# Optimization experiments

Hardware: AMD Instinct MI355X
Metric: run time of the kernel (lower is better)

## Reference

```python
import jax, jax.numpy as jnp
import numpy as np

N = 8192        # nodes
E = 262144      # edges (avg degree 32)
IN_CH = 256
CH = 128
SLOPE = 0.2     # PyG GATv2Conv default negative_slope


def gatv2(x, src, dst, wl, wr, att, b):
    """Single-head GATv2Conv (PyG defaults: share_weights=False, self-loops
    already appended to src/dst). x: [N, in]; wl, wr: [out, in]; att: [out]."""
    xl = x @ wl.T                      # [N, out] source-side transform (x_j)
    xr = x @ wr.T                      # [N, out] target-side transform (x_i)
    # per-edge attention logit: att . LeakyReLU(x_l[src] + x_r[dst])
    e = jax.nn.leaky_relu(xl[src] + xr[dst], SLOPE) @ att   # [E']
    # segment softmax over incoming edges of each target node
    m = jax.ops.segment_max(e, dst, num_segments=N)
    p = jnp.exp(e - m[dst])
    s = jax.ops.segment_sum(p, dst, num_segments=N)
    alpha = p / s[dst]                 # every node has a self-loop -> s > 0
    out = jax.ops.segment_sum(alpha[:, None] * xl[src], dst, num_segments=N)
    return out + b


def setup_inputs() -> dict:
    key = jax.random.key(0)
    ks = jax.random.split(key, 2 + 5 * 3)
    inp = {
        "x": jax.random.normal(ks[0], (N, IN_CH), dtype=jnp.float32),
        "edge_index": jax.random.randint(ks[1], (2, E), 0, N, dtype=jnp.int64),
    }
    dims = [(CH, IN_CH), (2 * CH, CH), (CH, 2 * CH), (CH, 2 * CH), (IN_CH, CH)]
    ki = 2
    for i, (oc, ic) in enumerate(dims, start=1):
        sc = (2.0 / (ic + oc)) ** 0.5  # glorot-ish
        inp[f"w{i}l"] = jax.random.normal(ks[ki], (oc, ic), dtype=jnp.float32) * sc
        inp[f"w{i}r"] = jax.random.normal(ks[ki + 1], (oc, ic), dtype=jnp.float32) * sc
        inp[f"a{i}"] = jax.random.normal(ks[ki + 2], (oc,), dtype=jnp.float32) * sc
        inp[f"b{i}"] = jnp.zeros((oc,), dtype=jnp.float32)
        ki += 3
    return inp


def reference(x, edge_index,
              w1l, w1r, a1, b1,
              w2l, w2r, a2, b2,
              w3l, w3r, a3, b3,
              w4l, w4r, a4, b4,
              w5l, w5r, a5, b5):
    loops = jnp.arange(N, dtype=edge_index.dtype)
    src = jnp.concatenate([edge_index[0], loops])   # add_self_loops=True
    dst = jnp.concatenate([edge_index[1], loops])
    h = jax.nn.relu(gatv2(x, src, dst, w1l, w1r, a1, b1))          # [N, CH]
    z = jax.nn.relu(gatv2(h, src, dst, w2l, w2r, a2, b2))          # [N, 2CH]
    re = jax.nn.relu(gatv2(z, src, dst, w3l, w3r, a3, b3))         # [N, CH]
    recon_edge = jax.nn.sigmoid(re @ re.T)                         # [N, N]
    xd = jax.nn.relu(gatv2(z, src, dst, w4l, w4r, a4, b4))         # [N, CH]
    x_rec = jax.nn.relu(gatv2(xd, src, dst, w5l, w5r, a5, b5))     # [N, IN_CH]
    return recon_edge, x_rec, z
```

## Files before the change

### kernel.cpp

```cpp
#include <hip/hip_runtime.h>
#include <hip/hip_bf16.h>
#include <math.h>

#define N_NODES 8192
#define N_EDGES 262144
#define EP (N_EDGES + N_NODES)
#define SLOPE 0.2f

typedef short bf16x8 __attribute__((ext_vector_type(8)));
typedef short short4v __attribute__((ext_vector_type(4)));
typedef float f32x4 __attribute__((ext_vector_type(4)));

__global__ void detect_i64(const int* __restrict__ raw, int* __restrict__ flag) {
    if (threadIdx.x == 0 && blockIdx.x == 0) {
        int acc = 0;
        for (int i = 0; i < 64; ++i) acc |= raw[2 * i + 1];
        *flag = (acc == 0) ? 1 : 0;
    }
}

__global__ void extract_edges(const int* __restrict__ raw, const int* __restrict__ flag,
                              int* __restrict__ esrc, int* __restrict__ edst) {
    int k = blockIdx.x * blockDim.x + threadIdx.x;
    if (k >= N_EDGES) return;
    if (*flag) {
        esrc[k] = raw[2 * (size_t)k];
        edst[k] = raw[2 * ((size_t)N_EDGES + k)];
    } else {
        esrc[k] = raw[k];
        edst[k] = raw[N_EDGES + k];
    }
}

__global__ void hist_k(const int* __restrict__ edst, int* __restrict__ counts) {
    int k = blockIdx.x * blockDim.x + threadIdx.x;
    if (k >= EP) return;
    int d = (k < N_EDGES) ? edst[k] : (k - N_EDGES);
    atomicAdd(&counts[d], 1);
}

__global__ void scan_k(const int* __restrict__ counts, int* __restrict__ row_ptr) {
    __shared__ int part[256];
    int t = threadIdx.x;
    int base = t * 32;
    int loc[32];
    int s = 0;
    for (int i = 0; i < 32; ++i) { loc[i] = s; s += counts[base + i]; }
    part[t] = s;
    __syncthreads();
    for (int off = 1; off < 256; off <<= 1) {
        int tmp = (t >= off) ? part[t - off] : 0;
        __syncthreads();
        part[t] += tmp;
        __syncthreads();
    }
    int incl = part[t];
    int excl = incl - s;
    for (int i = 0; i < 32; ++i) row_ptr[base + i] = excl + loc[i];
    if (t == 255) row_ptr[N_NODES] = incl;
}

__global__ void scatter_k(const int* __restrict__ esrc, const int* __restrict__ edst,
                          const int* __restrict__ row_ptr, int* __restrict__ cursor,
                          int* __restrict__ ssrc) {
    int k = blockIdx.x * blockDim.x + threadIdx.x;
    if (k >= EP) return;
    int s, d;
    if (k < N_EDGES) { s = esrc[k]; d = edst[k]; }
    else             { s = d = k - N_EDGES; }
    int pos = row_ptr[d] + atomicAdd(&cursor[d], 1);
    ssrc[pos] = s;
}

__global__ void cvt_f32_bf16(const float* __restrict__ in, unsigned short* __restrict__ out, int n) {
    int i = blockIdx.x * blockDim.x + threadIdx.x;
    if (i < n) {
        __hip_bfloat16 h = __float2bfloat16(in[i]);
        out[i] = *(unsigned short*)&h;
    }
}

__global__ void split3(const float* __restrict__ in, short* __restrict__ out, int logK) {
    int K = 1 << logK;
    int total = (N_NODES << logK) >> 2;
    int i = blockIdx.x * blockDim.x + threadIdx.x;
    if (i >= total) return;
    int r = i >> (logK - 2);
    int c4 = (i & ((1 << (logK - 2)) - 1)) << 2;
    f32x4 a = *(const f32x4*)&in[((size_t)r << logK) + c4];
    short4v h4, l4;
#pragma unroll
    for (int j = 0; j < 4; ++j) {
        __hip_bfloat16 hb = __float2bfloat16(a[j]);
        float hf = __bfloat162float(hb);
        __hip_bfloat16 lb = __float2bfloat16(a[j] - hf);
        h4[j] = *(short*)&hb;
        l4[j] = *(short*)&lb;
    }
    size_t ro = (size_t)r * (3 << logK);
    *(short4v*)&out[ro + c4] = h4;
    *(short4v*)&out[ro + K + c4] = l4;
    *(short4v*)&out[ro + 2 * K + c4] = h4;
}

__global__ void prep_w3(const float* __restrict__ wl, const float* __restrict__ wr,
                        short* __restrict__ out, int OC, int logK) {
    int K = 1 << logK;
    int i = blockIdx.x * blockDim.x + threadIdx.x;
    if (i >= ((OC << 1) << logK)) return;
    int r = i >> logK, c = i & (K - 1);
    float a = (r < OC) ? wl[((size_t)r << logK) + c]
                       : wr[((size_t)(r - OC) << logK) + c];
    __hip_bfloat16 hb = __float2bfloat16(a);
    float hf = __bfloat162float(hb);
    __hip_bfloat16 lb = __float2bfloat16(a - hf);
    short hs = *(short*)&hb, lo = *(short*)&lb;
    size_t ro = (size_t)r * 3 * K;
    out[ro + c] = hs;
    out[ro + K + c] = hs;
    out[ro + 2 * K + c] = lo;
}

#if __has_builtin(__builtin_amdgcn_global_load_lds)
#define GL16(gsrc, lbase, lofs)                                                       \
    __builtin_amdgcn_global_load_lds((const __attribute__((address_space(1))) void*)(gsrc), \
                                     (__attribute__((address_space(3))) void*)(lbase), 16, 0, 0)
#else
#define GL16(gsrc, lbase, lofs) (*(bf16x8*)((lbase) + (lofs)) = *(const bf16x8*)(gsrc))
#endif

__global__ __launch_bounds__(256) void gemm_bf16_nt(const short* __restrict__ A3,
                                                    const short* __restrict__ W3,
                                                    float* __restrict__ C,
                                                    int K3, int N2) {
    __shared__ __align__(16) short As[4096];
    __shared__ __align__(16) short Bs[4096];
    int tid = threadIdx.x;
    int gx = gridDim.x;
    int lgx = (gx == 8) ? 3 : 2;
    int orig = blockIdx.x + (blockIdx.y << lgx);
    int nwg = gx << 7;
    int swzb = (orig & 7) * (nwg >> 3) + (orig >> 3);
    int bx = swzb & (gx - 1), by = swzb >> lgx;
    int i0 = by * 64, j0 = bx * 64;

    int wave = tid >> 6, lane = tid & 63;
    int b0 = wave * 1024 + lane * 16;
    int row0 = b0 >> 7;
    int rb0 = b0 & 127;
    int scb = rb0 ^ ((row0 & 7) << 4);
    const short* gA0 = A3 + (size_t)(i0 + row0) * K3 + (scb >> 1);
    const short* gA1 = A3 + (size_t)(i0 + row0 + 32) * K3 + (scb >> 1);
    const short* gB0 = W3 + (size_t)(j0 + row0) * K3 + (scb >> 1);
    const short* gB1 = W3 + (size_t)(j0 + row0 + 32) * K3 + (scb >> 1);
    short* lA0 = As + wave * 512;
    short* lA1 = As + 2048 + wave * 512;
    short* lB0 = Bs + wave * 512;
    short* lB1 = Bs + 2048 + wave * 512;
    int lofs = lane * 8;

    int wr = (wave >> 1) * 32, wc = (wave & 1) * 32;
    int lm = lane & 15, quad = lane >> 4;
    f32x4 acc[2][2] = {};
    for (int k0 = 0; k0 < K3; k0 += 64) {
        GL16(gA0 + k0, lA0, lofs);
        GL16(gA1 + k0, lA1, lofs);
        GL16(gB0 + k0, lB0, lofs);
        GL16(gB1 + k0, lB1, lofs);
        __syncthreads();
#pragma unroll
        for (int ks = 0; ks < 2; ++ks) {
            int kb = ks * 64 + quad * 16;
            bf16x8 a[2], b[2];
#pragma unroll
            for (int u = 0; u < 2; ++u) {
                int r = wr + u * 16 + lm;
                a[u] = *(const bf16x8*)((const char*)As + ((((r << 7) | kb)) ^ ((r & 7) << 4)));
            }
#pragma unroll
            for (int v = 0; v < 2; ++v) {
                int r = wc + v * 16 + lm;
                b[v] = *(const bf16x8*)((const char*)Bs + ((((r << 7) | kb)) ^ ((r & 7) << 4)));
            }
#pragma unroll
            for (int u = 0; u < 2; ++u)
#pragma unroll
                for (int v = 0; v < 2; ++v)
                    acc[u][v] = __builtin_amdgcn_mfma_f32_16x16x32_bf16(a[u], b[v], acc[u][v], 0, 0, 0);
        }
        __syncthreads();
    }
#pragma unroll
    for (int u = 0; u < 2; ++u)
#pragma unroll
        for (int v = 0; v < 2; ++v)
#pragma unroll
            for (int r = 0; r < 4; ++r) {
                int row = i0 + wr + u * 16 + quad * 4 + r;
                int col = j0 + wc + v * 16 + lm;
                C[(size_t)row * N2 + col] = acc[u][v][r];
            }
}

#define LSTR 136

__global__ __launch_bounds__(256) void recon_mfma(const unsigned short* __restrict__ Rb,
                                                  float* __restrict__ C) {
    __shared__ __align__(16) short As[128 * LSTR];
    __shared__ __align__(16) short Bs[128 * LSTR];
    int tid = threadIdx.x;
    int orig = blockIdx.x + blockIdx.y * 64;
    int swzb = (orig & 7) * 512 + (orig >> 3);
    int bx = swzb & 63, by = swzb >> 6;
    int i0 = by * 128, j0 = bx * 128;
    const short* R = (const short*)Rb;
#pragma unroll
    for (int c = 0; c < 8; ++c) {
        int idx = tid + c * 256;
        int row = idx >> 4, col = (idx & 15) * 8;
        *(bf16x8*)(&As[row * LSTR + col]) = *(const bf16x8*)(&R[(size_t)(i0 + row) * 128 + col]);
        *(bf16x8*)(&Bs[row * LSTR + col]) = *(const bf16x8*)(&R[(size_t)(j0 + row) * 128 + col]);
    }
    __syncthreads();
    int wave = tid >> 6, lane = tid & 63;
    int wr = (wave >> 1) * 64, wc = (wave & 1) * 64;
    int lm = lane & 15, quad = lane >> 4;
    f32x4 acc[4][4] = {};
#pragma unroll
    for (int ks = 0; ks < 4; ++ks) {
        int ko = ks * 32 + quad * 8;
        bf16x8 a[4], b[4];
#pragma unroll
        for (int u = 0; u < 4; ++u)
            a[u] = *(const bf16x8*)(&As[(wr + u * 16 + lm) * LSTR + ko]);
#pragma unroll
        for (int v = 0; v < 4; ++v)
            b[v] = *(const bf16x8*)(&Bs[(wc + v * 16 + lm) * LSTR + ko]);
#pragma unroll
        for (int u = 0; u < 4; ++u)
#pragma unroll
            for (int v = 0; v < 4; ++v)
                acc[u][v] = __builtin_amdgcn_mfma_f32_16x16x32_bf16(a[u], b[v], acc[u][v], 0, 0, 0);
    }
#pragma unroll
    for (int u = 0; u < 4; ++u)
#pragma unroll
        for (int v = 0; v < 4; ++v)
#pragma unroll
            for (int r = 0; r < 4; ++r) {
                int row = i0 + wr + u * 16 + quad * 4 + r;
                int col = j0 + wc + v * 16 + lm;
                float val = acc[u][v][r];
                C[(size_t)row * 8192 + col] = 1.0f / (1.0f + __expf(-val));
            }
}

__global__ __launch_bounds__(256) void gat_node256(const int* __restrict__ row_ptr,
                                                   const int* __restrict__ ssrc,
                                                   const float* __restrict__ XLR,
                                                   const float* __restrict__ att,
                                                   const float* __restrict__ bias,
                                                   float* __restrict__ outp) {
    __shared__ float sacc[4][256];
    __shared__ float sm[4], ss[4];
    int d = blockIdx.x, t = threadIdx.x;
    int lane = t & 63, wave = t >> 6;
    int beg = row_ptr[d], end = row_ptr[d + 1];
    f32x4 xr = *(const f32x4*)&XLR[(size_t)d * 512 + 256 + lane * 4];
    f32x4 at = *(const f32x4*)&att[lane * 4];
    float m = -INFINITY, s = 0.0f;
    f32x4 acc = {0.0f, 0.0f, 0.0f, 0.0f};
    for (int p = beg + wave; p < end; p += 4) {
        int si = ssrc[p];
        f32x4 v = *(const f32x4*)&XLR[(size_t)si * 512 + lane * 4];
        float e = 0.0f;
#pragma unroll
        for (int j = 0; j < 4; ++j) {
            float u = v[j] + xr[j];
            u = (u > 0.0f) ? u : SLOPE * u;
            e += u * at[j];
        }
#pragma unroll
        for (int off = 32; off; off >>= 1) e += __shfl_xor(e, off, 64);
        float mn = fmaxf(m, e);
        float f = __expf(m - mn), p0 = __expf(e - mn);
        s = s * f + p0;
#pragma unroll
        for (int j = 0; j < 4; ++j) acc[j] = acc[j] * f + p0 * v[j];
        m = mn;
    }
    *(f32x4*)&sacc[wave][lane * 4] = acc;
    if (lane == 0) { sm[wave] = m; ss[wave] = s; }
    __syncthreads();
    float M = fmaxf(fmaxf(sm[0], sm[1]), fmaxf(sm[2], sm[3]));
    float tot = 0.0f, st = 0.0f;
#pragma unroll
    for (int w = 0; w < 4; ++w) {
        float fw = __expf(sm[w] - M);
        tot += sacc[w][t] * fw;
        st += ss[w] * fw;
    }
    outp[(size_t)d * 256 + t] = fmaxf(tot / st + bias[t], 0.0f);
}

__global__ __launch_bounds__(256) void gat_node128(const int* __restrict__ row_ptr,
                                                   const int* __restrict__ ssrc,
                                                   const float* __restrict__ XLR,
                                                   const float* __restrict__ att,
                                                   const float* __restrict__ bias,
                                                   float* __restrict__ outp) {
    __shared__ float sacc[8][128];
    __shared__ float sm[8], ss[8];
    int d = blockIdx.x, t = threadIdx.x;
    int ln = t & 31, hw = t >> 5;
    int beg = row_ptr[d], end = row_ptr[d + 1];
    f32x4 xr = *(const f32x4*)&XLR[(size_t)d * 256 + 128 + ln * 4];
    f32x4 at = *(const f32x4*)&att[ln * 4];
    float m = -INFINITY, s = 0.0f;
    f32x4 acc = {0.0f, 0.0f, 0.0f, 0.0f};
    for (int p = beg + hw; p < end; p += 8) {
        int si = ssrc[p];
        f32x4 v = *(const f32x4*)&XLR[(size_t)si * 256 + ln * 4];
        float e = 0.0f;
#pragma unroll
        for (int j = 0; j < 4; ++j) {
            float u = v[j] + xr[j];
            u = (u > 0.0f) ? u : SLOPE * u;
            e += u * at[j];
        }
#pragma unroll
        for (int off = 16; off; off >>= 1) e += __shfl_xor(e, off, 32);
        float mn = fmaxf(m, e);
        float f = __expf(m - mn), p0 = __expf(e - mn);
        s = s * f + p0;
#pragma unroll
        for (int j = 0; j < 4; ++j) acc[j] = acc[j] * f + p0 * v[j];
        m = mn;
    }
    *(f32x4*)&sacc[hw][ln * 4] = acc;
    if (ln == 0) { sm[hw] = m; ss[hw] = s; }
    __syncthreads();
    if (t < 128) {
        float M = sm[0];
#pragma unroll
        for (int w = 1; w < 8; ++w) M = fmaxf(M, sm[w]);
        float tot = 0.0f, st = 0.0f;
#pragma unroll
        for (int w = 0; w < 8; ++w) {
            float fw = __expf(sm[w] - M);
            tot += sacc[w][t] * fw;
            st += ss[w] * fw;
        }
        outp[(size_t)d * 128 + t] = fmaxf(tot / st + bias[t], 0.0f);
    }
}

static inline int ceil_div(int a, int b) { return (a + b - 1) / b; }

extern "C" void kernel_launch(void* const* d_in, const int* in_sizes, int n_in,
                              void* d_out, int out_size, void* d_ws, size_t ws_size,
                              hipStream_t stream) {
    const float* x    = (const float*)d_in[0];
    const int*   eraw = (const int*)d_in[1];

    const float* wl[5], *wr[5], *att[5], *bia[5];
    for (int l = 0; l < 5; ++l) {
        wl[l]  = (const float*)d_in[2 + 4 * l + 0];
        wr[l]  = (const float*)d_in[2 + 4 * l + 1];
        att[l] = (const float*)d_in[2 + 4 * l + 2];
        bia[l] = (const float*)d_in[2 + 4 * l + 3];
    }
    const int och[5]  = {128, 256, 128, 128, 256};
    const int logK[5] = {8, 7, 8, 8, 7};

    float* outp  = (float*)d_out;
    float* recon = outp;
    float* xrec  = outp + (size_t)67108864;
    float* zout  = outp + (size_t)69206016;

    float* W = (float*)d_ws;
    float* XLR   = W;
    float* hbuf  = W + 4194304;
    float* rebuf = W + 5242880;
    float* xdbuf = W + 6291456;
    short* A3    = (short*)(W + 7340032);
    short* W3    = (short*)(W + 10485760);
    unsigned short* Rb = (unsigned short*)(W + 10682368);
    int* I       = (int*)(W + 11206656);
    int* counts  = I;
    int* cursor  = I + 8192;
    int* row_ptr = I + 16384;
    int* ssrc    = I + 24577;
    int* esrc    = I + 294913;
    int* edst    = I + 557057;
    int* flag    = I + 819201;

    detect_i64<<<1, 64, 0, stream>>>(eraw, flag);
    extract_edges<<<ceil_div(N_EDGES, 256), 256, 0, stream>>>(eraw, flag, esrc, edst);
    hipMemsetAsync(counts, 0, 2 * 8192 * sizeof(int), stream);
    hist_k<<<ceil_div(EP, 256), 256, 0, stream>>>(edst, counts);
    scan_k<<<1, 256, 0, stream>>>(counts, row_ptr);
    scatter_k<<<ceil_div(EP, 256), 256, 0, stream>>>(esrc, edst, row_ptr, cursor, ssrc);

    const float* lin[5] = {x,    hbuf, zout,  zout,  xdbuf};
    float*       lof[5] = {hbuf, zout, rebuf, xdbuf, xrec };

    for (int l = 0; l < 5; ++l) {
        int lk = logK[l], OC = och[l];
        int N2 = OC << 1, K3 = 3 << lk;

        if (l != 3) {
            int tot = (N_NODES << lk) >> 2;
            split3<<<ceil_div(tot, 256), 256, 0, stream>>>(lin[l], A3, lk);
        }
        prep_w3<<<ceil_div(N2 << lk, 256), 256, 0, stream>>>(wl[l], wr[l], W3, OC, lk);

        dim3 g(N2 / 64, N_NODES / 64);
        gemm_bf16_nt<<<g, 256, 0, stream>>>(A3, W3, XLR, K3, N2);

        if (OC == 128)
            gat_node128<<<N_NODES, 256, 0, stream>>>(row_ptr, ssrc, XLR, att[l], bia[l], lof[l]);
        else
            gat_node256<<<N_NODES, 256, 0, stream>>>(row_ptr, ssrc, XLR, att[l], bia[l], lof[l]);

        if (l == 2) {
            cvt_f32_bf16<<<ceil_div(N_NODES * 128, 256), 256, 0, stream>>>(rebuf, Rb, N_NODES * 128);
            dim3 gr(64, 64);
            recon_mfma<<<gr, 256, 0, stream>>>(Rb, recon);
        }
    }
}
```

Measured before the change: 612.9 us.

## Fuse activation splitting into GAT epilogues, batch weight prep, double-buffer GEMM

Each GAT node kernel now writes the bf16 hi/lo/hi split of its output directly into the next layer's GEMM operand, and the recon bf16 copy. This removes the separate split3 and cvt passes and the fp32 intermediate buffers. Edge extraction is merged with the histogram, and self-loop counts move into the scan. All five weight preps run in one launch up front. The GEMM double-buffers its LDS tiles so the next K-tile load overlaps the MFMAs, and it writes XL and XR as separate arrays. The cost is more complex buffer-lifetime reasoning across layers and more LDS per GEMM block.

```diff
diff --git a/kernel.cpp b/kernel.cpp
--- a/kernel.cpp
+++ b/kernel.cpp
@@ -19,23 +19,21 @@
     }
 }
 
-__global__ void extract_edges(const int* __restrict__ raw, const int* __restrict__ flag,
-                              int* __restrict__ esrc, int* __restrict__ edst) {
+__global__ void extract_hist(const int* __restrict__ raw, const int* __restrict__ flag,
+                             int* __restrict__ esrc, int* __restrict__ edst,
+                             int* __restrict__ counts) {
     int k = blockIdx.x * blockDim.x + threadIdx.x;
     if (k >= N_EDGES) return;
+    int s, d;
     if (*flag) {
-        esrc[k] = raw[2 * (size_t)k];
-        edst[k] = raw[2 * ((size_t)N_EDGES + k)];
+        s = raw[2 * (size_t)k];
+        d = raw[2 * ((size_t)N_EDGES + k)];
     } else {
-        esrc[k] = raw[k];
-        edst[k] = raw[N_EDGES + k];
-    }
-}
-
-__global__ void hist_k(const int* __restrict__ edst, int* __restrict__ counts) {
-    int k = blockIdx.x * blockDim.x + threadIdx.x;
-    if (k >= EP) return;
-    int d = (k < N_EDGES) ? edst[k] : (k - N_EDGES);
+        s = raw[k];
+        d = raw[N_EDGES + k];
+    }
+    esrc[k] = s;
+    edst[k] = d;
     atomicAdd(&counts[d], 1);
 }
 
@@ -45,7 +43,7 @@
     int base = t * 32;
     int loc[32];
     int s = 0;
-    for (int i = 0; i < 32; ++i) { loc[i] = s; s += counts[base + i]; }
+    for (int i = 0; i < 32; ++i) { loc[i] = s; s += counts[base + i] + 1; }
     part[t] = s;
     __syncthreads();
     for (int off = 1; off < 256; off <<= 1) {
@@ -72,14 +70,6 @@
     ssrc[pos] = s;
 }
 
-__global__ void cvt_f32_bf16(const float* __restrict__ in, unsigned short* __restrict__ out, int n) {
-    int i = blockIdx.x * blockDim.x + threadIdx.x;
-    if (i < n) {
-        __hip_bfloat16 h = __float2bfloat16(in[i]);
-        out[i] = *(unsigned short*)&h;
-    }
-}
-
 __global__ void split3(const float* __restrict__ in, short* __restrict__ out, int logK) {
     int K = 1 << logK;
     int total = (N_NODES << logK) >> 2;
@@ -103,19 +93,29 @@
     *(short4v*)&out[ro + 2 * K + c4] = h4;
 }
 
-__global__ void prep_w3(const float* __restrict__ wl, const float* __restrict__ wr,
-                        short* __restrict__ out, int OC, int logK) {
-    int K = 1 << logK;
-    int i = blockIdx.x * blockDim.x + threadIdx.x;
-    if (i >= ((OC << 1) << logK)) return;
-    int r = i >> logK, c = i & (K - 1);
-    float a = (r < OC) ? wl[((size_t)r << logK) + c]
-                       : wr[((size_t)(r - OC) << logK) + c];
+struct WPrep {
+    const float* wl[5];
+    const float* wr[5];
+    int oc[5];
+    int lk[5];
+};
+
+__global__ void prep_w3_all(WPrep P, short* __restrict__ out) {
+    int gid = blockIdx.x * blockDim.x + threadIdx.x;
+    int l = gid >> 16;
+    if (l >= 5) return;
+    int rem = gid & 65535;
+    int lk = P.lk[l], K = 1 << lk;
+    int r = rem >> lk, c = rem & (K - 1);
+    int OC = P.oc[l];
+    const float* w = (r < OC) ? P.wl[l] : P.wr[l];
+    int rr = (r < OC) ? r : r - OC;
+    float a = w[((size_t)rr << lk) + c];
     __hip_bfloat16 hb = __float2bfloat16(a);
     float hf = __bfloat162float(hb);
     __hip_bfloat16 lb = __float2bfloat16(a - hf);
     short hs = *(short*)&hb, lo = *(short*)&lb;
-    size_t ro = (size_t)r * 3 * K;
+    size_t ro = (size_t)l * 196608 + (size_t)r * 3 * K;
     out[ro + c] = hs;
     out[ro + K + c] = hs;
     out[ro + 2 * K + c] = lo;
@@ -131,10 +131,11 @@
 
 __global__ __launch_bounds__(256) void gemm_bf16_nt(const short* __restrict__ A3,
                                                     const short* __restrict__ W3,
-                                                    float* __restrict__ C,
-                                                    int K3, int N2) {
-    __shared__ __align__(16) short As[4096];
-    __shared__ __align__(16) short Bs[4096];
+                                                    float* __restrict__ XL,
+                                                    float* __restrict__ XR,
+                                                    int K3, int N2, int OC) {
+    __shared__ __align__(16) short As[2][4096];
+    __shared__ __align__(16) short Bs[2][4096];
     int tid = threadIdx.x;
     int gx = gridDim.x;
     int lgx = (gx == 8) ? 3 : 2;
@@ -153,21 +154,33 @@
     const short* gA1 = A3 + (size_t)(i0 + row0 + 32) * K3 + (scb >> 1);
     const short* gB0 = W3 + (size_t)(j0 + row0) * K3 + (scb >> 1);
     const short* gB1 = W3 + (size_t)(j0 + row0 + 32) * K3 + (scb >> 1);
-    short* lA0 = As + wave * 512;
-    short* lA1 = As + 2048 + wave * 512;
-    short* lB0 = Bs + wave * 512;
-    short* lB1 = Bs + 2048 + wave * 512;
     int lofs = lane * 8;
+
+#define STAGE(pb, k0s)                                      \
+    do {                                                    \
+        GL16(gA0 + (k0s), &As[pb][wave * 512], lofs);       \
+        GL16(gA1 + (k0s), &As[pb][2048 + wave * 512], lofs);\
+        GL16(gB0 + (k0s), &Bs[pb][wave * 512], lofs);       \
+        GL16(gB1 + (k0s), &Bs[pb][2048 + wave * 512], lofs);\
+    } while (0)
 
     int wr = (wave >> 1) * 32, wc = (wave & 1) * 32;
     int lm = lane & 15, quad = lane >> 4;
     f32x4 acc[2][2] = {};
-    for (int k0 = 0; k0 < K3; k0 += 64) {
-        GL16(gA0 + k0, lA0, lofs);
-        GL16(gA1 + k0, lA1, lofs);
-        GL16(gB0 + k0, lB0, lofs);
-        GL16(gB1 + k0, lB1, lofs);
-        __syncthreads();
+    int nt = K3 >> 6;
+    STAGE(0, 0);
+    int cur = 0;
+    for (int t = 0; t < nt; ++t) {
+        if (t + 1 < nt) {
+            STAGE(cur ^ 1, (t + 1) << 6);
+            asm volatile("s_waitcnt vmcnt(4)" ::: "memory");
+        } else {
+            asm volatile("s_waitcnt vmcnt(0)" ::: "memory");
+        }
+        __builtin_amdgcn_s_barrier();
+        __builtin_amdgcn_sched_barrier(0);
+        const char* Ab = (const char*)&As[cur][0];
+        const char* Bb = (const char*)&Bs[cur][0];
 #pragma unroll
         for (int ks = 0; ks < 2; ++ks) {
             int kb = ks * 64 + quad * 16;
@@ -175,12 +188,12 @@
 #pragma unroll
             for (int u = 0; u < 2; ++u) {
                 int r = wr + u * 16 + lm;
-                a[u] = *(const bf16x8*)((const char*)As + ((((r << 7) | kb)) ^ ((r & 7) << 4)));
+                a[u] = *(const bf16x8*)(Ab + (((r << 7) | kb) ^ ((r & 7) << 4)));
             }
 #pragma unroll
             for (int v = 0; v < 2; ++v) {
                 int r = wc + v * 16 + lm;
-                b[v] = *(const bf16x8*)((const char*)Bs + ((((r << 7) | kb)) ^ ((r & 7) << 4)));
+                b[v] = *(const bf16x8*)(Bb + (((r << 7) | kb) ^ ((r & 7) << 4)));
             }
 #pragma unroll
             for (int u = 0; u < 2; ++u)
@@ -188,8 +201,14 @@
                 for (int v = 0; v < 2; ++v)
                     acc[u][v] = __builtin_amdgcn_mfma_f32_16x16x32_bf16(a[u], b[v], acc[u][v], 0, 0, 0);
         }
-        __syncthreads();
-    }
+        __builtin_amdgcn_sched_barrier(0);
+        __builtin_amdgcn_s_barrier();
+        cur ^= 1;
+    }
+#undef STAGE
+    float* Cb;
+    int col0;
+    if (j0 < OC) { Cb = XL; col0 = j0; } else { Cb = XR; col0 = j0 - OC; }
 #pragma unroll
     for (int u = 0; u < 2; ++u)
 #pragma unroll
@@ -197,8 +216,8 @@
 #pragma unroll
             for (int r = 0; r < 4; ++r) {
                 int row = i0 + wr + u * 16 + quad * 4 + r;
-                int col = j0 + wc + v * 16 + lm;
-                C[(size_t)row * N2 + col] = acc[u][v][r];
+                int col = col0 + wc + v * 16 + lm;
+                Cb[(size_t)row * OC + col] = acc[u][v][r];
             }
 }
 
@@ -257,22 +276,24 @@
 
 __global__ __launch_bounds__(256) void gat_node256(const int* __restrict__ row_ptr,
                                                    const int* __restrict__ ssrc,
-                                                   const float* __restrict__ XLR,
+                                                   const float* __restrict__ XL,
+                                                   const float* __restrict__ XR,
                                                    const float* __restrict__ att,
                                                    const float* __restrict__ bias,
-                                                   float* __restrict__ outp) {
+                                                   float* __restrict__ outf,
+                                                   short* __restrict__ a3) {
     __shared__ float sacc[4][256];
     __shared__ float sm[4], ss[4];
     int d = blockIdx.x, t = threadIdx.x;
     int lane = t & 63, wave = t >> 6;
     int beg = row_ptr[d], end = row_ptr[d + 1];
-    f32x4 xr = *(const f32x4*)&XLR[(size_t)d * 512 + 256 + lane * 4];
+    f32x4 xr = *(const f32x4*)&XR[(size_t)d * 256 + lane * 4];
     f32x4 at = *(const f32x4*)&att[lane * 4];
     float m = -INFINITY, s = 0.0f;
     f32x4 acc = {0.0f, 0.0f, 0.0f, 0.0f};
     for (int p = beg + wave; p < end; p += 4) {
         int si = ssrc[p];
-        f32x4 v = *(const f32x4*)&XLR[(size_t)si * 512 + lane * 4];
+        f32x4 v = *(const f32x4*)&XL[(size_t)si * 256 + lane * 4];
         float e = 0.0f;
 #pragma unroll
         for (int j = 0; j < 4; ++j) {
@@ -300,27 +321,40 @@
         tot += sacc[w][t] * fw;
         st += ss[w] * fw;
     }
-    outp[(size_t)d * 256 + t] = fmaxf(tot / st + bias[t], 0.0f);
+    float val = fmaxf(tot / st + bias[t], 0.0f);
+    if (outf) outf[(size_t)d * 256 + t] = val;
+    if (a3) {
+        __hip_bfloat16 hb = __float2bfloat16(val);
+        float hf = __bfloat162float(hb);
+        __hip_bfloat16 lb = __float2bfloat16(val - hf);
+        size_t ro = (size_t)d * 768;
+        a3[ro + t] = *(short*)&hb;
+        a3[ro + 256 + t] = *(short*)&lb;
+        a3[ro + 512 + t] = *(short*)&hb;
+    }
 }
 
 __global__ __launch_bounds__(256) void gat_node128(const int* __restrict__ row_ptr,
                                                    const int* __restrict__ ssrc,
-                                                   const float* __restrict__ XLR,
+                                                   const float* __restrict__ XL,
+                                                   const float* __restrict__ XR,
                                                    const float* __restrict__ att,
                                                    const float* __restrict__ bias,
-                                                   float* __restrict__ outp) {
+                                                   float* __restrict__ outf,
+                                                   short* __restrict__ a3,
+                                                   unsigned short* __restrict__ rb) {
     __shared__ float sacc[8][128];
     __shared__ float sm[8], ss[8];
     int d = blockIdx.x, t = threadIdx.x;
     int ln = t & 31, hw = t >> 5;
     int beg = row_ptr[d], end = row_ptr[d + 1];
-    f32x4 xr = *(const f32x4*)&XLR[(size_t)d * 256 + 128 + ln * 4];
+    f32x4 xr = *(const f32x4*)&XR[(size_t)d * 128 + ln * 4];
     f32x4 at = *(const f32x4*)&att[ln * 4];
     float m = -INFINITY, s = 0.0f;
     f32x4 acc = {0.0f, 0.0f, 0.0f, 0.0f};
     for (int p = beg + hw; p < end; p += 8) {
         int si = ssrc[p];
-        f32x4 v = *(const f32x4*)&XLR[(size_t)si * 256 + ln * 4];
+        f32x4 v = *(const f32x4*)&XL[(size_t)si * 128 + ln * 4];
         float e = 0.0f;
 #pragma unroll
         for (int j = 0; j < 4; ++j) {
@@ -351,7 +385,21 @@
             tot += sacc[w][t] * fw;
             st += ss[w] * fw;
         }
-        outp[(size_t)d * 128 + t] = fmaxf(tot / st + bias[t], 0.0f);
+        float val = fmaxf(tot / st + bias[t], 0.0f);
+        if (outf) outf[(size_t)d * 128 + t] = val;
+        if (a3) {
+            __hip_bfloat16 hb = __float2bfloat16(val);
+            float hf = __bfloat162float(hb);
+            __hip_bfloat16 lb = __float2bfloat16(val - hf);
+            size_t ro = (size_t)d * 384;
+            a3[ro + t] = *(short*)&hb;
+            a3[ro + 128 + t] = *(short*)&lb;
+            a3[ro + 256 + t] = *(short*)&hb;
+        }
+        if (rb) {
+            __hip_bfloat16 hb = __float2bfloat16(val);
+            rb[d * 128 + t] = *(unsigned short*)&hb;
+        }
     }
 }
 
@@ -363,15 +411,18 @@
     const float* x    = (const float*)d_in[0];
     const int*   eraw = (const int*)d_in[1];
 
-    const float* wl[5], *wr[5], *att[5], *bia[5];
+    WPrep P;
+    const float* att[5];
+    const float* bia[5];
     for (int l = 0; l < 5; ++l) {
-        wl[l]  = (const float*)d_in[2 + 4 * l + 0];
-        wr[l]  = (const float*)d_in[2 + 4 * l + 1];
-        att[l] = (const float*)d_in[2 + 4 * l + 2];
-        bia[l] = (const float*)d_in[2 + 4 * l + 3];
+        P.wl[l] = (const float*)d_in[2 + 4 * l + 0];
+        P.wr[l] = (const float*)d_in[2 + 4 * l + 1];
+        att[l]  = (const float*)d_in[2 + 4 * l + 2];
+        bia[l]  = (const float*)d_in[2 + 4 * l + 3];
     }
     const int och[5]  = {128, 256, 128, 128, 256};
     const int logK[5] = {8, 7, 8, 8, 7};
+    for (int l = 0; l < 5; ++l) { P.oc[l] = och[l]; P.lk[l] = logK[l]; }
 
     float* outp  = (float*)d_out;
     float* recon = outp;
@@ -379,14 +430,12 @@
     float* zout  = outp + (size_t)69206016;
 
     float* W = (float*)d_ws;
-    float* XLR   = W;
-    float* hbuf  = W + 4194304;
-    float* rebuf = W + 5242880;
-    float* xdbuf = W + 6291456;
-    short* A3    = (short*)(W + 7340032);
-    short* W3    = (short*)(W + 10485760);
-    unsigned short* Rb = (unsigned short*)(W + 10682368);
-    int* I       = (int*)(W + 11206656);
+    float* XL    = W;
+    float* XR    = W + 2097152;
+    short* A3    = (short*)(W + 4194304);
+    short* W3all = (short*)(W + 7340032);
+    unsigned short* Rb = (unsigned short*)(W + 7831552);
+    int* I       = (int*)(W + 8355840);
     int* counts  = I;
     int* cursor  = I + 8192;
     int* row_ptr = I + 16384;
@@ -395,36 +444,34 @@
     int* edst    = I + 557057;
     int* flag    = I + 819201;
 
+    hipMemsetAsync(counts, 0, 2 * 8192 * sizeof(int), stream);
     detect_i64<<<1, 64, 0, stream>>>(eraw, flag);
-    extract_edges<<<ceil_div(N_EDGES, 256), 256, 0, stream>>>(eraw, flag, esrc, edst);
-    hipMemsetAsync(counts, 0, 2 * 8192 * sizeof(int), stream);
-    hist_k<<<ceil_div(EP, 256), 256, 0, stream>>>(edst, counts);
+    extract_hist<<<ceil_div(N_EDGES, 256), 256, 0, stream>>>(eraw, flag, esrc, edst, counts);
     scan_k<<<1, 256, 0, stream>>>(counts, row_ptr);
     scatter_k<<<ceil_div(EP, 256), 256, 0, stream>>>(esrc, edst, row_ptr, cursor, ssrc);
 
-    const float* lin[5] = {x,    hbuf, zout,  zout,  xdbuf};
-    float*       lof[5] = {hbuf, zout, rebuf, xdbuf, xrec };
+    prep_w3_all<<<1280, 256, 0, stream>>>(P, W3all);
+    split3<<<ceil_div(N_NODES * 256 / 4, 256), 256, 0, stream>>>(x, A3, 8);
 
     for (int l = 0; l < 5; ++l) {
         int lk = logK[l], OC = och[l];
         int N2 = OC << 1, K3 = 3 << lk;
 
-        if (l != 3) {
-            int tot = (N_NODES << lk) >> 2;
-            split3<<<ceil_div(tot, 256), 256, 0, stream>>>(lin[l], A3, lk);
-        }
-        prep_w3<<<ceil_div(N2 << lk, 256), 256, 0, stream>>>(wl[l], wr[l], W3, OC, lk);
-
         dim3 g(N2 / 64, N_NODES / 64);
-        gemm_bf16_nt<<<g, 256, 0, stream>>>(A3, W3, XLR, K3, N2);
-
-        if (OC == 128)
-            gat_node128<<<N_NODES, 256, 0, stream>>>(row_ptr, ssrc, XLR, att[l], bia[l], lof[l]);
-        else
-            gat_node256<<<N_NODES, 256, 0, stream>>>(row_ptr, ssrc, XLR, att[l], bia[l], lof[l]);
+        gemm_bf16_nt<<<g, 256, 0, stream>>>(A3, W3all + (size_t)l * 196608, XL, XR, K3, N2, OC);
+
+        if (OC == 128) {
+            float* of = nullptr;
+            short* a3 = (l == 0 || l == 3) ? A3 : nullptr;
+            unsigned short* rb = (l == 2) ? Rb : nullptr;
+            gat_node128<<<N_NODES, 256, 0, stream>>>(row_ptr, ssrc, XL, XR, att[l], bia[l], of, a3, rb);
+        } else {
+            float* of = (l == 1) ? zout : xrec;
+            short* a3 = (l == 1) ? A3 : nullptr;
+            gat_node256<<<N_NODES, 256, 0, stream>>>(row_ptr, ssrc, XL, XR, att[l], bia[l], of, a3);
+        }
 
         if (l == 2) {
-            cvt_f32_bf16<<<ceil_div(N_NODES * 128, 256), 256, 0, stream>>>(rebuf, Rb, N_NODES * 128);
             dim3 gr(64, 64);
             recon_mfma<<<gr, 256, 0, stream>>>(Rb, recon);
         }
```

After: 596.2 us. 1.03x faster.
